# Kernel tuning notes

Hardware: AMD Instinct MI355X
Metric: run time of the kernel (lower is better)

The kernel has to match this reference:

```python
import jax, jax.numpy as jnp
import numpy as np

B, N, E, DIN, DOUT = 8, 4096, 160, 15, 15


def _mha(q, k, v, in_w, in_b, out_w, out_b, h):
    # torch.nn.MultiheadAttention math: packed in_proj, per-head scaled dot attn, out_proj.
    e = q.shape[-1]
    d = e // h
    scale = 1.0 / np.sqrt(d)

    def proj(x, w, b):
        y = x @ w.T + b
        return jnp.moveaxis(y.reshape(y.shape[:-1] + (h, d)), -2, -3)  # [..., h, L, d]

    qh = proj(q, in_w[:e], in_b[:e])
    kh = proj(k, in_w[e:2 * e], in_b[e:2 * e])
    vh = proj(v, in_w[2 * e:], in_b[2 * e:])
    a = jax.nn.softmax(jnp.einsum('...hld,...hmd->...hlm', qh, kh) * scale, axis=-1)
    o = jnp.einsum('...hlm,...hmd->...hld', a, vh)
    o = jnp.moveaxis(o, -3, -2).reshape(q.shape)
    return o @ out_w.T + out_b


def _attn_layer(seq, Wq, Wk, Wv, in_w, in_b, out_w, out_b, h):
    # AttentionLayer: extra Wq/Wk/Wv projections feeding the MHA
    return _mha(seq @ Wq, seq @ Wk, seq @ Wv, in_w, in_b, out_w, out_b, h)


def setup_inputs():
    key = jax.random.key(0)
    ks = jax.random.split(key, 20)
    s = 1.0 / np.sqrt(E)
    p = lambda i, shape: jax.random.normal(ks[i], shape, dtype=jnp.float32) * s
    return {
        'X_batch': jax.random.normal(ks[0], (B, N, E), dtype=jnp.float32),
        'in_idx': jax.random.randint(ks[1], (B, N, DIN), 0, N),
        'out_idx': jax.random.randint(ks[2], (B, N, DOUT), 0, N),
        'iWq': p(3, (E, E)), 'iWk': p(4, (E, E)), 'iWv': p(5, (E, E)),
        'i_in_w': p(6, (3 * E, E)), 'i_in_b': jnp.zeros(3 * E, jnp.float32),
        'i_out_w': p(7, (E, E)), 'i_out_b': jnp.zeros(E, jnp.float32),
        'oWq': p(8, (E, E)), 'oWk': p(9, (E, E)), 'oWv': p(10, (E, E)),
        'o_in_w': p(11, (3 * E, E)), 'o_in_b': jnp.zeros(3 * E, jnp.float32),
        'o_out_w': p(12, (E, E)), 'o_out_b': jnp.zeros(E, jnp.float32),
        'f_in_w': p(13, (3 * E, E)), 'f_in_b': jnp.zeros(3 * E, jnp.float32),
        'f_out_w': p(14, (E, E)), 'f_out_b': jnp.zeros(E, jnp.float32),
        'lin_w': p(15, (E, E)), 'lin_b': jnp.zeros(E, jnp.float32),
    }


def reference(X_batch, in_idx, out_idx,
              iWq, iWk, iWv, i_in_w, i_in_b, i_out_w, i_out_b,
              oWq, oWk, oWv, o_in_w, o_in_b, o_out_w, o_out_b,
              f_in_w, f_in_b, f_out_w, f_out_b, lin_w, lin_b):
    b_ix = jnp.arange(X_batch.shape[0])[:, None, None]
    self_f = X_batch[:, :, None, :]                                   # [B,N,1,E]
    seq_in = jnp.concatenate([self_f, X_batch[b_ix, in_idx]], axis=2)  # [B,N,1+DIN,E]
    seq_out = jnp.concatenate([self_f, X_batch[b_ix, out_idx]], axis=2)
    a_in = _attn_layer(seq_in, iWq, iWk, iWv, i_in_w, i_in_b, i_out_w, i_out_b, 5)
    a_out = _attn_layer(seq_out, oWq, oWk, oWv, o_in_w, o_in_b, o_out_w, o_out_b, 5)
    a = jnp.concatenate([a_in, a_out], axis=2)                         # [B,N,2+DIN+DOUT,E]
    f = _mha(a, a, a, f_in_w, f_in_b, f_out_w, f_out_b, 1)
    pooled = jnp.max(f, axis=2)                                        # max over sequence dim
    return jax.nn.elu(pooled @ lin_w.T + lin_b)
```

## Files before the change

kernel.cpp:

```cpp
#include <hip/hip_runtime.h>
#include <hip/hip_bf16.h>
#include <math.h>

#define NTH 256

typedef __bf16 bf16x8 __attribute__((ext_vector_type(8)));
typedef float  f32x4  __attribute__((ext_vector_type(4)));
typedef unsigned short ushort;
typedef ushort u16x8 __attribute__((ext_vector_type(8)));

__device__ __forceinline__ ushort f2bf(float x){
    union { float f; unsigned int u; } v; v.f = x;
    unsigned int r = v.u + 0x7fffu + ((v.u >> 16) & 1u);
    return (ushort)(r >> 16);
}
__device__ __forceinline__ float bf2f(ushort h){
    union { unsigned int u; float f; } v; v.u = ((unsigned int)h) << 16;
    return v.f;
}

__global__ void prep_combined_bf(const float* __restrict__ Wq, const float* __restrict__ Wk,
                                 const float* __restrict__ Wv, const float* __restrict__ in_w,
                                 ushort* __restrict__ dh)
{
    int o = blockIdx.x*NTH + threadIdx.x;
    if (o >= 76800) return;
    int c = o/160, j = o - c*160;
    const float* Wsel = (c<160) ? Wq : (c<320) ? Wk : Wv;
    const float* wrow = Wsel + j*160;
    const float* irow = in_w + c*160;
    float s = 0.f;
    for (int k=0;k<160;k++) s = fmaf(wrow[k], irow[k], s);
    dh[o] = f2bf(s);
}

__global__ void prep_H_split(const float* __restrict__ f_in_w, const float* __restrict__ out_w,
                             ushort* __restrict__ dh, float* __restrict__ tmp)
{
    int o = blockIdx.x*NTH + threadIdx.x;
    if (o >= 76800) return;
    int n = o/160, k = o - n*160;
    float s = 0.f;
    for (int c=0;c<160;c++) s = fmaf(f_in_w[n*160+c], out_w[c*160+k], s);
    if (n < 320) dh[o] = f2bf(s);
    else         tmp[(n-320)*160 + k] = s;
}

__global__ void prep_H_fold(const float* __restrict__ fo, const float* __restrict__ Hv,
                            ushort* __restrict__ dh)
{
    int o = blockIdx.x*NTH + threadIdx.x;
    if (o >= 25600) return;
    int n = o/160, k = o - n*160;
    float s = 0.f;
    for (int j=0;j<160;j++) s = fmaf(fo[n*160+j], Hv[j*160+k], s);
    dh[(320+n)*160 + k] = f2bf(s);
}

__global__ void prep_cvec(const float* __restrict__ f_in_w, const float* __restrict__ out_b,
                          const float* __restrict__ f_in_b, float* __restrict__ cvt)
{
    int n = blockIdx.x*NTH + threadIdx.x;
    if (n >= 480) return;
    float s = f_in_b[n];
    for (int c=0;c<160;c++) s = fmaf(f_in_w[n*160+c], out_b[c], s);
    cvt[n] = s;
}

__global__ void prep_cvec_fold(const float* __restrict__ fo, const float* __restrict__ cvt,
                               float* __restrict__ cv)
{
    int n = blockIdx.x*NTH + threadIdx.x;
    if (n >= 480) return;
    if (n < 320){ cv[n] = cvt[n]; return; }
    int m = n - 320;
    float s = 0.f;
    for (int j=0;j<160;j++) s = fmaf(fo[m*160+j], cvt[320+j], s);
    cv[n] = s;
}

__global__ void prep_conv_bf1(const float* __restrict__ src, ushort* __restrict__ dh, int n)
{
    int o = blockIdx.x*NTH + threadIdx.x;
    if (o >= n) return;
    dh[o] = f2bf(src[o]);
}

__global__ void prep_conv_bf2(const float* __restrict__ src,
                              ushort* __restrict__ dh, ushort* __restrict__ dl, int n)
{
    int o = blockIdx.x*NTH + threadIdx.x;
    if (o >= n) return;
    float s = src[o];
    ushort h = f2bf(s);
    dh[o] = h; dl[o] = f2bf(s - bf2f(h));
}

__global__ __launch_bounds__(NTH)
void gemm_mfma_lin(const float* __restrict__ A,
                   const ushort* __restrict__ Wh, const ushort* __restrict__ Wl,
                   const float* __restrict__ bias, float* __restrict__ C, int N)
{
    __shared__ ushort sAh[128*40], sAl[128*40];
    __shared__ ushort sWh[160*40], sWl[160*40];

    const int tid = threadIdx.x;
    const int lane = tid & 63, wave = tid >> 6;
    const int wm = wave >> 1, wn = wave & 1;
    const int ln = lane & 15, g = lane >> 4;
    const long m0 = (long)blockIdx.x * 128;
    const int  n0 = blockIdx.y * 160;

    f32x4 acc[4][5];
#pragma unroll
    for (int mt=0;mt<4;mt++)
#pragma unroll
        for (int nt=0;nt<5;nt++)
#pragma unroll
            for (int r=0;r<4;r++) acc[mt][nt][r] = 0.f;

    for (int k0=0;k0<160;k0+=32){
#pragma unroll
        for (int i=0;i<4;i++){
            int f = tid + 256*i;
            int m = f >> 3, seg = f & 7;
            float4 v = *(const float4*)(A + (m0+m)*160 + k0 + seg*4);
            ushort4 hv, lv;
            hv.x = f2bf(v.x); lv.x = f2bf(v.x - bf2f(hv.x));
            hv.y = f2bf(v.y); lv.y = f2bf(v.y - bf2f(hv.y));
            hv.z = f2bf(v.z); lv.z = f2bf(v.z - bf2f(hv.z));
            hv.w = f2bf(v.w); lv.w = f2bf(v.w - bf2f(hv.w));
            *(ushort4*)(sAh + m*40 + seg*4) = hv;
            *(ushort4*)(sAl + m*40 + seg*4) = lv;
        }
#pragma unroll
        for (int i=0;i<5;i++){
            int e = tid + 256*i;
            int pl = (e >= 640);
            int idx = pl ? e-640 : e;
            int n = idx >> 2, seg = idx & 3;
            const ushort* src = (pl ? Wl : Wh) + (long)(n0+n)*160 + k0 + seg*8;
            ushort* dst = (pl ? sWl : sWh) + n*40 + seg*8;
            *(uint4*)dst = *(const uint4*)src;
        }
        __syncthreads();

        bf16x8 ah[4], al[4];
#pragma unroll
        for (int mt=0;mt<4;mt++){
            int off = (wm*64 + mt*16 + ln)*40 + g*8;
            ah[mt] = *(const bf16x8*)(sAh + off);
            al[mt] = *(const bf16x8*)(sAl + off);
        }
#pragma unroll
        for (int nt=0;nt<5;nt++){
            int offw = (wn*80 + nt*16 + ln)*40 + g*8;
            bf16x8 bh = *(const bf16x8*)(sWh + offw);
            bf16x8 bl = *(const bf16x8*)(sWl + offw);
#pragma unroll
            for (int mt=0;mt<4;mt++){
                acc[mt][nt] = __builtin_amdgcn_mfma_f32_16x16x32_bf16(ah[mt], bh, acc[mt][nt], 0,0,0);
                acc[mt][nt] = __builtin_amdgcn_mfma_f32_16x16x32_bf16(al[mt], bh, acc[mt][nt], 0,0,0);
                acc[mt][nt] = __builtin_amdgcn_mfma_f32_16x16x32_bf16(ah[mt], bl, acc[mt][nt], 0,0,0);
            }
        }
        __syncthreads();
    }

#pragma unroll
    for (int nt=0;nt<5;nt++){
        int col = n0 + wn*80 + nt*16 + ln;
        float bv = bias[col];
#pragma unroll
        for (int mt=0;mt<4;mt++){
#pragma unroll
            for (int r=0;r<4;r++){
                long row = m0 + wm*64 + mt*16 + g*4 + r;
                float x = acc[mt][nt][r] + bv;
                x = x > 0.f ? x : expm1f(x);
                C[row*N + col] = x;
            }
        }
    }
}

__global__ __launch_bounds__(NTH)
void gemm_bf(const ushort* __restrict__ A0, const ushort* __restrict__ A1,
             const ushort* __restrict__ Wh0, const ushort* __restrict__ Wh1,
             const float* __restrict__ b0, const float* __restrict__ b1,
             ushort* __restrict__ C0, ushort* __restrict__ C1, int N)
{
    const int z = blockIdx.z;
    const ushort* A  = z ? A1 : A0;
    const ushort* Wh = z ? Wh1 : Wh0;
    const float* bias = z ? b1 : b0;
    ushort* C = z ? C1 : C0;

    __shared__ ushort sA[128*40];
    __shared__ ushort sW[160*40];

    const int tid = threadIdx.x;
    const int lane = tid & 63, wave = tid >> 6;
    const int wm = wave >> 1, wn = wave & 1;
    const int ln = lane & 15, g = lane >> 4;
    const long m0 = (long)blockIdx.x * 128;
    const int  n0 = blockIdx.y * 160;

    f32x4 acc[4][5];
#pragma unroll
    for (int mt=0;mt<4;mt++)
#pragma unroll
        for (int nt=0;nt<5;nt++)
#pragma unroll
            for (int r=0;r<4;r++) acc[mt][nt][r] = 0.f;

    for (int k0=0;k0<160;k0+=32){
#pragma unroll
        for (int i=0;i<2;i++){
            int e = tid + 256*i;
            int m = e >> 2, seg = e & 3;
            *(uint4*)(sA + m*40 + seg*8) =
                *(const uint4*)(A + (m0+m)*160 + k0 + seg*8);
        }
#pragma unroll
        for (int i=0;i<3;i++){
            int e = tid + 256*i;
            if (e < 640){
                int n = e >> 2, seg = e & 3;
                *(uint4*)(sW + n*40 + seg*8) =
                    *(const uint4*)(Wh + (long)(n0+n)*160 + k0 + seg*8);
            }
        }
        __syncthreads();

        bf16x8 af[4];
#pragma unroll
        for (int mt=0;mt<4;mt++)
            af[mt] = *(const bf16x8*)(sA + (wm*64 + mt*16 + ln)*40 + g*8);
#pragma unroll
        for (int nt=0;nt<5;nt++){
            bf16x8 bh = *(const bf16x8*)(sW + (wn*80 + nt*16 + ln)*40 + g*8);
#pragma unroll
            for (int mt=0;mt<4;mt++)
                acc[mt][nt] = __builtin_amdgcn_mfma_f32_16x16x32_bf16(af[mt], bh, acc[mt][nt], 0,0,0);
        }
        __syncthreads();
    }

#pragma unroll
    for (int nt=0;nt<5;nt++){
        int col = n0 + wn*80 + nt*16 + ln;
        float bv = bias[col];
#pragma unroll
        for (int mt=0;mt<4;mt++){
#pragma unroll
            for (int r=0;r<4;r++){
                long row = m0 + wm*64 + mt*16 + g*4 + r;
                C[row*N + col] = f2bf(acc[mt][nt][r] + bv);
            }
        }
    }
}

__global__ __launch_bounds__(64)
void attn_layer_mfma(const ushort* __restrict__ XPi, const ushort* __restrict__ XPo,
                     const int* __restrict__ in_idx, const int* __restrict__ out_idx,
                     ushort* __restrict__ Oi, ushort* __restrict__ Oo, int node_base)
{
    const ushort* XP = blockIdx.y ? XPo : XPi;
    const int*  idx  = blockIdx.y ? out_idx : in_idx;
    ushort* O        = blockIdx.y ? Oo : Oi;

    __shared__ ushort XPg[16*496];
    __shared__ ushort Pall[5*16*24];

    const int lane = threadIdx.x;
    const int ln = lane & 15, q = lane >> 4;
    const int node = node_base + blockIdx.x;
    const int bb = node >> 12, nn = node & 4095;

    int idxv = nn;
    if (lane >= 1 && lane < 16) idxv = idx[(long)node*15 + lane-1];

#pragma unroll
    for (int i=0;i<15;i++){
        int e = lane + 64*i;
        int r = e/60, c = e - r*60;
        int rowg = __shfl(idxv, r);
        *(uint4*)(XPg + r*496 + c*8) =
            *(const uint4*)(XP + (long)(bb*4096 + rowg)*480 + c*8);
    }
    __syncthreads();

    const float scale = 0.17677669529663687f;
#pragma unroll
    for (int h=0;h<5;h++){
        bf16x8 ka = *(const bf16x8*)(XPg + ln*496 + 160 + h*32 + q*8);
        bf16x8 qb = *(const bf16x8*)(XPg + ln*496 +       h*32 + q*8);
        f32x4 s = {0.f,0.f,0.f,0.f};
        s = __builtin_amdgcn_mfma_f32_16x16x32_bf16(ka, qb, s, 0,0,0);
        float x[4], m = -1e30f;
#pragma unroll
        for (int r=0;r<4;r++){ x[r] = s[r]*scale; m = fmaxf(m, x[r]); }
        m = fmaxf(m, __shfl_xor(m, 16));
        m = fmaxf(m, __shfl_xor(m, 32));
        float e0[4], sum = 0.f;
#pragma unroll
        for (int r=0;r<4;r++){ e0[r] = __expf(x[r]-m); sum += e0[r]; }
        sum += __shfl_xor(sum, 16);
        sum += __shfl_xor(sum, 32);
        float inv = 1.f/sum;
        ushort4 pw;
        pw.x = f2bf(e0[0]*inv); pw.y = f2bf(e0[1]*inv);
        pw.z = f2bf(e0[2]*inv); pw.w = f2bf(e0[3]*inv);
        *(ushort4*)(Pall + h*384 + ln*24 + q*4) = pw;
    }
    __syncthreads();

#pragma unroll
    for (int h=0;h<5;h++){
        u16x8 ta;
#pragma unroll
        for (int jj=0;jj<8;jj++) ta[jj] = 0;
        if (q < 2) ta = *(const u16x8*)(Pall + h*384 + ln*24 + q*8);
        bf16x8 ap = *(bf16x8*)&ta;
#pragma unroll
        for (int half=0; half<2; half++){
            u16x8 tb;
#pragma unroll
            for (int jj=0;jj<8;jj++) tb[jj] = 0;
            if (q < 2){
#pragma unroll
                for (int jj=0;jj<8;jj++)
                    tb[jj] = XPg[(q*8+jj)*496 + 320 + h*32 + half*16 + ln];
            }
            bf16x8 bv = *(bf16x8*)&tb;
            f32x4 o = {0.f,0.f,0.f,0.f};
            o = __builtin_amdgcn_mfma_f32_16x16x32_bf16(ap, bv, o, 0,0,0);
#pragma unroll
            for (int r=0;r<4;r++)
                O[(long)(blockIdx.x*16 + q*4 + r)*160 + h*32 + half*16 + ln] = f2bf(o[r]);
        }
    }
}

__global__ __launch_bounds__(512)
void fused_fq_attn_pool(const ushort* __restrict__ O_i, const ushort* __restrict__ O_o,
                        const ushort* __restrict__ Hi, const ushort* __restrict__ Ho,
                        const float* __restrict__ c_i, const float* __restrict__ c_o,
                        const float* __restrict__ fb, float* __restrict__ pooled,
                        int node_base)
{
    __shared__ ushort sFQ[4*32*328];
    __shared__ ushort sVt[4*160*40];
    __shared__ ushort sP [4*32*40];

    const int tid  = threadIdx.x;
    const int lane = tid & 63, wave = tid >> 6;
    const int ln = lane & 15, g = lane >> 4;
    const int wl = wave >> 2, wn = wave & 3;
    const int nl0 = blockIdx.x * 4;

    const ushort* Ow = wl ? O_o : O_i;
    const ushort* Hw = wl ? Ho  : Hi;
    const float*  cw = wl ? c_o : c_i;

    bf16x8 ofr[4][5];
#pragma unroll
    for (int nd=0; nd<4; nd++)
#pragma unroll
        for (int kc=0; kc<5; kc++)
            ofr[nd][kc] = *(const bf16x8*)(Ow + ((long)(nl0+nd)*16 + ln)*160 + kc*32 + g*8);

    bf16x8 hf[5], hn[5];
#pragma unroll
    for (int kc=0; kc<5; kc++)
        hf[kc] = *(const bf16x8*)(Hw + (long)(wn*16 + ln)*160 + kc*32 + g*8);

    for (int t=0; t<8; t++){
        const int cg  = t*4 + wn;
        const int cgn = cg + 4;
        if (t < 7 && cgn < 30){
            const ushort* hrow = Hw + (long)(cgn*16 + ln)*160;
#pragma unroll
            for (int kc=0; kc<5; kc++)
                hn[kc] = *(const bf16x8*)(hrow + kc*32 + g*8);
        }

        if (cg < 30){
            f32x4 acc[4];
#pragma unroll
            for (int nd=0; nd<4; nd++)
#pragma unroll
                for (int r=0;r<4;r++) acc[nd][r] = 0.f;

#pragma unroll
            for (int kc=0; kc<5; kc++)
#pragma unroll
                for (int nd=0; nd<4; nd++)
                    acc[nd] = __builtin_amdgcn_mfma_f32_16x16x32_bf16(hf[kc], ofr[nd][kc], acc[nd], 0,0,0);

            const int cb0 = cg*16 + g*4;
            float4 cb = *(const float4*)(cw + cb0);
            if (cg < 20){
#pragma unroll
                for (int nd=0; nd<4; nd++){
                    ushort4 w4;
                    w4.x = f2bf(acc[nd][0] + cb.x);
                    w4.y = f2bf(acc[nd][1] + cb.y);
                    w4.z = f2bf(acc[nd][2] + cb.z);
                    w4.w = f2bf(acc[nd][3] + cb.w);
                    *(ushort4*)(sFQ + nd*10496 + (wl*16 + ln)*328 + cb0) = w4;
                }
            } else {
                const int c0 = cb0 - 320;
#pragma unroll
                for (int nd=0; nd<4; nd++){
                    sVt[nd*6400 + (c0+0)*40 + wl*16 + ln] = f2bf(acc[nd][0] + cb.x);
                    sVt[nd*6400 + (c0+1)*40 + wl*16 + ln] = f2bf(acc[nd][1] + cb.y);
                    sVt[nd*6400 + (c0+2)*40 + wl*16 + ln] = f2bf(acc[nd][2] + cb.z);
                    sVt[nd*6400 + (c0+3)*40 + wl*16 + ln] = f2bf(acc[nd][3] + cb.w);
                }
            }
        }
#pragma unroll
        for (int kc=0; kc<5; kc++) hf[kc] = hn[kc];
    }
    __syncthreads();

    const int nd = wave >> 1, th = wave & 1;
    const ushort* myQ = sFQ + nd*10496;
    const ushort* myV = sVt + nd*6400;
    ushort*       myP = sP  + nd*1280;

    f32x4 sc[2];
#pragma unroll
    for (int tj=0; tj<2; tj++){
        f32x4 a = {0.f,0.f,0.f,0.f};
#pragma unroll
        for (int kc=0; kc<5; kc++){
            bf16x8 ka = *(const bf16x8*)(myQ + (tj*16+ln)*328 + 160 + kc*32 + g*8);
            bf16x8 qb = *(const bf16x8*)(myQ + (th*16+ln)*328 +       kc*32 + g*8);
            a = __builtin_amdgcn_mfma_f32_16x16x32_bf16(ka, qb, a, 0,0,0);
        }
        sc[tj] = a;
    }

    const float scale = 0.07905694150420949f;
    {
        float x[2][4], m = -1e30f;
#pragma unroll
        for (int tj=0; tj<2; tj++)
#pragma unroll
            for (int r=0;r<4;r++){ x[tj][r] = sc[tj][r]*scale; m = fmaxf(m, x[tj][r]); }
        m = fmaxf(m, __shfl_xor(m, 16));
        m = fmaxf(m, __shfl_xor(m, 32));
        float sum = 0.f;
#pragma unroll
        for (int tj=0; tj<2; tj++)
#pragma unroll
            for (int r=0;r<4;r++){ x[tj][r] = __expf(x[tj][r]-m); sum += x[tj][r]; }
        sum += __shfl_xor(sum, 16);
        sum += __shfl_xor(sum, 32);
        float inv = 1.f/sum;
#pragma unroll
        for (int tj=0; tj<2; tj++){
            ushort4 pw;
            pw.x = f2bf(x[tj][0]*inv); pw.y = f2bf(x[tj][1]*inv);
            pw.z = f2bf(x[tj][2]*inv); pw.w = f2bf(x[tj][3]*inv);
            *(ushort4*)(myP + (th*16+ln)*40 + tj*16 + g*4) = pw;
        }
    }
    __syncthreads();

    bf16x8 ap[2];
#pragma unroll
    for (int mi=0; mi<2; mi++)
        ap[mi] = *(const bf16x8*)(myP + (mi*16+ln)*40 + g*8);

    const long node = (long)node_base + nl0 + nd;
#pragma unroll
    for (int nt5=0; nt5<5; nt5++){
        const int nt = th*5 + nt5;
        bf16x8 bv = *(const bf16x8*)(myV + (nt*16+ln)*40 + g*8);
        float vmax = -1e30f;
#pragma unroll
        for (int mi=0; mi<2; mi++){
            f32x4 o = {0.f,0.f,0.f,0.f};
            o = __builtin_amdgcn_mfma_f32_16x16x32_bf16(ap[mi], bv, o, 0,0,0);
#pragma unroll
            for (int r=0;r<4;r++) vmax = fmaxf(vmax, o[r]);
        }
        vmax = fmaxf(vmax, __shfl_xor(vmax, 16));
        vmax = fmaxf(vmax, __shfl_xor(vmax, 32));
        if (g == 0){
            int col = nt*16 + ln;
            pooled[node*160 + col] = vmax + fb[col];
        }
    }
}

extern "C" void kernel_launch(void* const* d_in, const int* in_sizes, int n_in,
                              void* d_out, int out_size, void* d_ws, size_t ws_size,
                              hipStream_t stream)
{
    const float* X       = (const float*)d_in[0];
    const int*   in_idx  = (const int*)  d_in[1];
    const int*   out_idx = (const int*)  d_in[2];
    const float* iWq     = (const float*)d_in[3];
    const float* iWk     = (const float*)d_in[4];
    const float* iWv     = (const float*)d_in[5];
    const float* i_in_w  = (const float*)d_in[6];
    const float* i_in_b  = (const float*)d_in[7];
    const float* i_out_w = (const float*)d_in[8];
    const float* i_out_b = (const float*)d_in[9];
    const float* oWq     = (const float*)d_in[10];
    const float* oWk     = (const float*)d_in[11];
    const float* oWv     = (const float*)d_in[12];
    const float* o_in_w  = (const float*)d_in[13];
    const float* o_in_b  = (const float*)d_in[14];
    const float* o_out_w = (const float*)d_in[15];
    const float* o_out_b = (const float*)d_in[16];
    const float* f_in_w  = (const float*)d_in[17];
    const float* f_in_b  = (const float*)d_in[18];
    const float* f_out_w = (const float*)d_in[19];
    const float* f_out_b = (const float*)d_in[20];
    const float* lin_w   = (const float*)d_in[21];
    const float* lin_b   = (const float*)d_in[22];

    float* ws = (float*)d_ws;
    float* pooled = ws;
    float* c_i    = pooled + 5242880;
    float* c_o    = c_i + 480;
    float* cvt_i  = c_o + 480;
    float* cvt_o  = cvt_i + 480;
    float* Hvt_i  = cvt_o + 480;
    float* Hvt_o  = Hvt_i + 25600;
    ushort* ub    = (ushort*)(Hvt_o + 25600);
    ushort* Xb    = ub;
    ushort* XPb_i = Xb + 5242880;
    ushort* XPb_o = XPb_i + 15728640;
    ushort* Wci_h = XPb_o + 15728640;
    ushort* Wco_h = Wci_h + 76800;
    ushort* Hi_h  = Wco_h + 76800;
    ushort* Ho_h  = Hi_h  + 76800;
    ushort* li_h  = Ho_h  + 76800;
    ushort* li_l  = li_h  + 25600;
    ushort* sb_us = li_l + 25600;
    const unsigned long long fixed = 23825280ULL;

    size_t avail = ws_size / 4;
    int ns = 32768;
    while (ns > 64 && fixed + 2560ULL*ns > avail) ns >>= 1;

    ushort* O_i = sb_us;
    ushort* O_o = O_i + (size_t)2560*ns;

    prep_combined_bf<<<300,NTH,0,stream>>>(iWq,iWk,iWv,i_in_w, Wci_h);
    prep_combined_bf<<<300,NTH,0,stream>>>(oWq,oWk,oWv,o_in_w, Wco_h);
    prep_H_split<<<300,NTH,0,stream>>>(f_in_w, i_out_w, Hi_h, Hvt_i);
    prep_H_split<<<300,NTH,0,stream>>>(f_in_w, o_out_w, Ho_h, Hvt_o);
    prep_H_fold<<<100,NTH,0,stream>>>(f_out_w, Hvt_i, Hi_h);
    prep_H_fold<<<100,NTH,0,stream>>>(f_out_w, Hvt_o, Ho_h);
    prep_cvec<<<2,NTH,0,stream>>>(f_in_w, i_out_b, f_in_b, cvt_i);
    prep_cvec<<<2,NTH,0,stream>>>(f_in_w, o_out_b, f_in_b, cvt_o);
    prep_cvec_fold<<<2,NTH,0,stream>>>(f_out_w, cvt_i, c_i);
    prep_cvec_fold<<<2,NTH,0,stream>>>(f_out_w, cvt_o, c_o);
    prep_conv_bf2<<<100,NTH,0,stream>>>(lin_w, li_h, li_l, 25600);
    prep_conv_bf1<<<20480,NTH,0,stream>>>(X, Xb, 5242880);

    dim3 g1(256, 3, 2);
    gemm_bf<<<g1,NTH,0,stream>>>(Xb, Xb, Wci_h, Wco_h, i_in_b, o_in_b,
                                 XPb_i, XPb_o, 480);

    int S = 32768 / ns;
    for (int s=0;s<S;s++){
        int base = s*ns;
        dim3 ga(ns, 2);
        attn_layer_mfma<<<ga,64,0,stream>>>(XPb_i, XPb_o, in_idx, out_idx, O_i, O_o, base);
        fused_fq_attn_pool<<<ns/4,512,0,stream>>>(O_i, O_o, Hi_h, Ho_h, c_i, c_o,
                                                  f_out_b, pooled, base);
    }

    dim3 g6(256, 1);
    gemm_mfma_lin<<<g6,NTH,0,stream>>>(pooled, li_h, li_l, lin_b, (float*)d_out, 160);
}
```

Baseline: 764.6 us.

## Fuse per-node attention layers and final attention-pool into one mega kernel

Merges the per-node gather+5-head attention kernel and the fused F/Q attention-pool kernel into a single 1024-thread block that handles 4 nodes. The intermediate O tensors now stay in LDS instead of going through global memory, and the out-layer gather is prefetched into registers while the in-layer is computed. The chunked launch loop and its O workspace are removed. The cost is a large LDS footprint (about 142 KB) and 1024-thread blocks, which limit occupancy to one block per CU, and half the waves sit idle in the final attention stage.

```diff
diff --git a/kernel.cpp b/kernel.cpp
--- a/kernel.cpp
+++ b/kernel.cpp
@@ -262,106 +262,133 @@
     }
 }
 
-__global__ __launch_bounds__(64)
-void attn_layer_mfma(const ushort* __restrict__ XPi, const ushort* __restrict__ XPo,
-                     const int* __restrict__ in_idx, const int* __restrict__ out_idx,
-                     ushort* __restrict__ Oi, ushort* __restrict__ Oo, int node_base)
-{
-    const ushort* XP = blockIdx.y ? XPo : XPi;
-    const int*  idx  = blockIdx.y ? out_idx : in_idx;
-    ushort* O        = blockIdx.y ? Oo : Oi;
-
-    __shared__ ushort XPg[16*496];
-    __shared__ ushort Pall[5*16*24];
-
-    const int lane = threadIdx.x;
-    const int ln = lane & 15, q = lane >> 4;
-    const int node = node_base + blockIdx.x;
-    const int bb = node >> 12, nn = node & 4095;
-
-    int idxv = nn;
-    if (lane >= 1 && lane < 16) idxv = idx[(long)node*15 + lane-1];
-
-#pragma unroll
-    for (int i=0;i<15;i++){
-        int e = lane + 64*i;
-        int r = e/60, c = e - r*60;
-        int rowg = __shfl(idxv, r);
-        *(uint4*)(XPg + r*496 + c*8) =
-            *(const uint4*)(XP + (long)(bb*4096 + rowg)*480 + c*8);
+__global__ __launch_bounds__(1024)
+void mega_node(const ushort* __restrict__ XPi, const ushort* __restrict__ XPo,
+               const int* __restrict__ in_idx, const int* __restrict__ out_idx,
+               const ushort* __restrict__ Hi, const ushort* __restrict__ Ho,
+               const float* __restrict__ c_i, const float* __restrict__ c_o,
+               const float* __restrict__ fb, float* __restrict__ pooled)
+{
+    __shared__ ushort lds[72704];
+
+    const int tid  = threadIdx.x;
+    const int lane = tid & 63, w = tid >> 6;
+    const int ln = lane & 15, g = lane >> 4;
+    const int nl0 = blockIdx.x * 4;
+
+    ushort* XPg = lds;
+    ushort* sO  = lds + 31744;
+    ushort* sPh = lds + 53248;
+
+    const int ndA = w & 3, p = w >> 2;
+    const int nodeA = nl0 + ndA;
+    const int bb = nodeA >> 12, nn = nodeA & 4095;
+    int idx0 = nn, idx1 = nn;
+    if (lane >= 1 && lane < 16){
+        idx0 = in_idx [(long)nodeA*15 + lane-1];
+        idx1 = out_idx[(long)nodeA*15 + lane-1];
+    }
+
+    uint4 l1r[4];
+#pragma unroll
+    for (int i=0;i<4;i++){
+        int e = i*256 + p*64 + lane;
+        if (e < 960){
+            int r = e/60, c = e - r*60;
+            int rowg = __shfl(idx0, r);
+            *(uint4*)(XPg + ndA*7936 + r*496 + c*8) =
+                *(const uint4*)(XPi + (long)(bb*4096 + rowg)*480 + c*8);
+        }
+    }
+#pragma unroll
+    for (int i=0;i<4;i++){
+        int e = i*256 + p*64 + lane;
+        if (e < 960){
+            int r = e/60, c = e - r*60;
+            int rowg = __shfl(idx1, r);
+            l1r[i] = *(const uint4*)(XPo + (long)(bb*4096 + rowg)*480 + c*8);
+        }
     }
     __syncthreads();
 
-    const float scale = 0.17677669529663687f;
-#pragma unroll
-    for (int h=0;h<5;h++){
-        bf16x8 ka = *(const bf16x8*)(XPg + ln*496 + 160 + h*32 + q*8);
-        bf16x8 qb = *(const bf16x8*)(XPg + ln*496 +       h*32 + q*8);
-        f32x4 s = {0.f,0.f,0.f,0.f};
-        s = __builtin_amdgcn_mfma_f32_16x16x32_bf16(ka, qb, s, 0,0,0);
-        float x[4], m = -1e30f;
-#pragma unroll
-        for (int r=0;r<4;r++){ x[r] = s[r]*scale; m = fmaxf(m, x[r]); }
-        m = fmaxf(m, __shfl_xor(m, 16));
-        m = fmaxf(m, __shfl_xor(m, 32));
-        float e0[4], sum = 0.f;
-#pragma unroll
-        for (int r=0;r<4;r++){ e0[r] = __expf(x[r]-m); sum += e0[r]; }
-        sum += __shfl_xor(sum, 16);
-        sum += __shfl_xor(sum, 32);
-        float inv = 1.f/sum;
-        ushort4 pw;
-        pw.x = f2bf(e0[0]*inv); pw.y = f2bf(e0[1]*inv);
-        pw.z = f2bf(e0[2]*inv); pw.w = f2bf(e0[3]*inv);
-        *(ushort4*)(Pall + h*384 + ln*24 + q*4) = pw;
-    }
-    __syncthreads();
-
-#pragma unroll
-    for (int h=0;h<5;h++){
-        u16x8 ta;
-#pragma unroll
-        for (int jj=0;jj<8;jj++) ta[jj] = 0;
-        if (q < 2) ta = *(const u16x8*)(Pall + h*384 + ln*24 + q*8);
-        bf16x8 ap = *(bf16x8*)&ta;
-#pragma unroll
-        for (int half=0; half<2; half++){
-            u16x8 tb;
-#pragma unroll
-            for (int jj=0;jj<8;jj++) tb[jj] = 0;
-            if (q < 2){
-#pragma unroll
-                for (int jj=0;jj<8;jj++)
-                    tb[jj] = XPg[(q*8+jj)*496 + 320 + h*32 + half*16 + ln];
-            }
-            bf16x8 bv = *(bf16x8*)&tb;
-            f32x4 o = {0.f,0.f,0.f,0.f};
-            o = __builtin_amdgcn_mfma_f32_16x16x32_bf16(ap, bv, o, 0,0,0);
-#pragma unroll
-            for (int r=0;r<4;r++)
-                O[(long)(blockIdx.x*16 + q*4 + r)*160 + h*32 + half*16 + ln] = f2bf(o[r]);
-        }
-    }
-}
-
-__global__ __launch_bounds__(512)
-void fused_fq_attn_pool(const ushort* __restrict__ O_i, const ushort* __restrict__ O_o,
-                        const ushort* __restrict__ Hi, const ushort* __restrict__ Ho,
-                        const float* __restrict__ c_i, const float* __restrict__ c_o,
-                        const float* __restrict__ fb, float* __restrict__ pooled,
-                        int node_base)
-{
-    __shared__ ushort sFQ[4*32*328];
-    __shared__ ushort sVt[4*160*40];
-    __shared__ ushort sP [4*32*40];
-
-    const int tid  = threadIdx.x;
-    const int lane = tid & 63, wave = tid >> 6;
-    const int ln = lane & 15, g = lane >> 4;
-    const int wl = wave >> 2, wn = wave & 3;
-    const int nl0 = blockIdx.x * 4;
-
-    const ushort* Ow = wl ? O_o : O_i;
+    const float scale1 = 0.17677669529663687f;
+#pragma unroll
+    for (int l=0; l<2; l++){
+        if (l == 1){
+#pragma unroll
+            for (int i=0;i<4;i++){
+                int e = i*256 + p*64 + lane;
+                if (e < 960){
+                    int r = e/60, c = e - r*60;
+                    *(uint4*)(XPg + ndA*7936 + r*496 + c*8) = l1r[i];
+                }
+            }
+            __syncthreads();
+        }
+
+#pragma unroll
+        for (int rep=0; rep<2; rep++){
+            int t = w + rep*16;
+            if (t < 20){
+                int nd = t/5, h = t - 5*(t/5);
+                const ushort* xg = XPg + nd*7936;
+                bf16x8 ka = *(const bf16x8*)(xg + ln*496 + 160 + h*32 + g*8);
+                bf16x8 qb = *(const bf16x8*)(xg + ln*496 +       h*32 + g*8);
+                f32x4 s = {0.f,0.f,0.f,0.f};
+                s = __builtin_amdgcn_mfma_f32_16x16x32_bf16(ka, qb, s, 0,0,0);
+                float x[4], m = -1e30f;
+#pragma unroll
+                for (int r=0;r<4;r++){ x[r] = s[r]*scale1; m = fmaxf(m, x[r]); }
+                m = fmaxf(m, __shfl_xor(m, 16));
+                m = fmaxf(m, __shfl_xor(m, 32));
+                float e0[4], sum = 0.f;
+#pragma unroll
+                for (int r=0;r<4;r++){ e0[r] = __expf(x[r]-m); sum += e0[r]; }
+                sum += __shfl_xor(sum, 16);
+                sum += __shfl_xor(sum, 32);
+                float inv = 1.f/sum;
+                ushort4 pw;
+                pw.x = f2bf(e0[0]*inv); pw.y = f2bf(e0[1]*inv);
+                pw.z = f2bf(e0[2]*inv); pw.w = f2bf(e0[3]*inv);
+                *(ushort4*)(sPh + t*384 + ln*24 + g*4) = pw;
+            }
+        }
+        __syncthreads();
+
+#pragma unroll
+        for (int rep=0; rep<2; rep++){
+            int t = w + rep*16;
+            if (t < 20){
+                int nd = t/5, h = t - 5*(t/5);
+                const ushort* xg = XPg + nd*7936;
+                u16x8 ta;
+#pragma unroll
+                for (int jj=0;jj<8;jj++) ta[jj] = 0;
+                if (g < 2) ta = *(const u16x8*)(sPh + t*384 + ln*24 + g*8);
+                bf16x8 ap = *(bf16x8*)&ta;
+#pragma unroll
+                for (int half=0; half<2; half++){
+                    u16x8 tb;
+#pragma unroll
+                    for (int jj=0;jj<8;jj++) tb[jj] = 0;
+                    if (g < 2){
+#pragma unroll
+                        for (int jj=0;jj<8;jj++)
+                            tb[jj] = xg[(g*8+jj)*496 + 320 + h*32 + half*16 + ln];
+                    }
+                    bf16x8 bv = *(bf16x8*)&tb;
+                    f32x4 o = {0.f,0.f,0.f,0.f};
+                    o = __builtin_amdgcn_mfma_f32_16x16x32_bf16(ap, bv, o, 0,0,0);
+#pragma unroll
+                    for (int r=0;r<4;r++)
+                        sO[((nd*2+l)*16 + g*4+r)*168 + h*32 + half*16 + ln] = f2bf(o[r]);
+                }
+            }
+        }
+        __syncthreads();
+    }
+
+    const int wl = w >> 3, wn = w & 7;
     const ushort* Hw = wl ? Ho  : Hi;
     const float*  cw = wl ? c_o : c_i;
 
@@ -370,21 +397,28 @@
     for (int nd=0; nd<4; nd++)
 #pragma unroll
         for (int kc=0; kc<5; kc++)
-            ofr[nd][kc] = *(const bf16x8*)(Ow + ((long)(nl0+nd)*16 + ln)*160 + kc*32 + g*8);
+            ofr[nd][kc] = *(const bf16x8*)(sO + ((nd*2+wl)*16 + ln)*168 + kc*32 + g*8);
 
     bf16x8 hf[5], hn[5];
 #pragma unroll
     for (int kc=0; kc<5; kc++)
         hf[kc] = *(const bf16x8*)(Hw + (long)(wn*16 + ln)*160 + kc*32 + g*8);
-
-    for (int t=0; t<8; t++){
-        const int cg  = t*4 + wn;
-        const int cgn = cg + 4;
-        if (t < 7 && cgn < 30){
-            const ushort* hrow = Hw + (long)(cgn*16 + ln)*160;
-#pragma unroll
-            for (int kc=0; kc<5; kc++)
-                hn[kc] = *(const bf16x8*)(hrow + kc*32 + g*8);
+    __syncthreads();
+
+    ushort* sFQ = lds;
+    ushort* sVt = lds + 41984;
+    ushort* sPf = lds + 67584;
+
+    for (int t=0; t<4; t++){
+        const int cg = t*8 + wn;
+        if (t < 3){
+            const int cgn = cg + 8;
+            if (cgn < 30){
+                const ushort* hrow = Hw + (long)(cgn*16 + ln)*160;
+#pragma unroll
+                for (int kc=0; kc<5; kc++)
+                    hn[kc] = *(const bf16x8*)(hrow + kc*32 + g*8);
+            }
         }
 
         if (cg < 30){
@@ -428,26 +462,26 @@
     }
     __syncthreads();
 
-    const int nd = wave >> 1, th = wave & 1;
+    const int nd = w >> 1, th = w & 1;
     const ushort* myQ = sFQ + nd*10496;
     const ushort* myV = sVt + nd*6400;
-    ushort*       myP = sP  + nd*1280;
-
-    f32x4 sc[2];
-#pragma unroll
-    for (int tj=0; tj<2; tj++){
-        f32x4 a = {0.f,0.f,0.f,0.f};
-#pragma unroll
-        for (int kc=0; kc<5; kc++){
-            bf16x8 ka = *(const bf16x8*)(myQ + (tj*16+ln)*328 + 160 + kc*32 + g*8);
-            bf16x8 qb = *(const bf16x8*)(myQ + (th*16+ln)*328 +       kc*32 + g*8);
-            a = __builtin_amdgcn_mfma_f32_16x16x32_bf16(ka, qb, a, 0,0,0);
-        }
-        sc[tj] = a;
-    }
-
-    const float scale = 0.07905694150420949f;
-    {
+    ushort*       myP = sPf + nd*1280;
+
+    if (w < 8){
+        f32x4 sc[2];
+#pragma unroll
+        for (int tj=0; tj<2; tj++){
+            f32x4 a = {0.f,0.f,0.f,0.f};
+#pragma unroll
+            for (int kc=0; kc<5; kc++){
+                bf16x8 ka = *(const bf16x8*)(myQ + (tj*16+ln)*328 + 160 + kc*32 + g*8);
+                bf16x8 qb = *(const bf16x8*)(myQ + (th*16+ln)*328 +       kc*32 + g*8);
+                a = __builtin_amdgcn_mfma_f32_16x16x32_bf16(ka, qb, a, 0,0,0);
+            }
+            sc[tj] = a;
+        }
+
+        const float scale = 0.07905694150420949f;
         float x[2][4], m = -1e30f;
 #pragma unroll
         for (int tj=0; tj<2; tj++)
@@ -473,29 +507,31 @@
     }
     __syncthreads();
 
-    bf16x8 ap[2];
-#pragma unroll
-    for (int mi=0; mi<2; mi++)
-        ap[mi] = *(const bf16x8*)(myP + (mi*16+ln)*40 + g*8);
-
-    const long node = (long)node_base + nl0 + nd;
-#pragma unroll
-    for (int nt5=0; nt5<5; nt5++){
-        const int nt = th*5 + nt5;
-        bf16x8 bv = *(const bf16x8*)(myV + (nt*16+ln)*40 + g*8);
-        float vmax = -1e30f;
-#pragma unroll
-        for (int mi=0; mi<2; mi++){
-            f32x4 o = {0.f,0.f,0.f,0.f};
-            o = __builtin_amdgcn_mfma_f32_16x16x32_bf16(ap[mi], bv, o, 0,0,0);
-#pragma unroll
-            for (int r=0;r<4;r++) vmax = fmaxf(vmax, o[r]);
-        }
-        vmax = fmaxf(vmax, __shfl_xor(vmax, 16));
-        vmax = fmaxf(vmax, __shfl_xor(vmax, 32));
-        if (g == 0){
-            int col = nt*16 + ln;
-            pooled[node*160 + col] = vmax + fb[col];
+    if (w < 8){
+        bf16x8 ap[2];
+#pragma unroll
+        for (int mi=0; mi<2; mi++)
+            ap[mi] = *(const bf16x8*)(myP + (mi*16+ln)*40 + g*8);
+
+        const long node = (long)nl0 + nd;
+#pragma unroll
+        for (int nt5=0; nt5<5; nt5++){
+            const int nt = th*5 + nt5;
+            bf16x8 bv = *(const bf16x8*)(myV + (nt*16+ln)*40 + g*8);
+            float vmax = -1e30f;
+#pragma unroll
+            for (int mi=0; mi<2; mi++){
+                f32x4 o = {0.f,0.f,0.f,0.f};
+                o = __builtin_amdgcn_mfma_f32_16x16x32_bf16(ap[mi], bv, o, 0,0,0);
+#pragma unroll
+                for (int r=0;r<4;r++) vmax = fmaxf(vmax, o[r]);
+            }
+            vmax = fmaxf(vmax, __shfl_xor(vmax, 16));
+            vmax = fmaxf(vmax, __shfl_xor(vmax, 32));
+            if (g == 0){
+                int col = nt*16 + ln;
+                pooled[node*160 + col] = vmax + fb[col];
+            }
         }
     }
 }
@@ -536,8 +572,7 @@
     float* cvt_o  = cvt_i + 480;
     float* Hvt_i  = cvt_o + 480;
     float* Hvt_o  = Hvt_i + 25600;
-    ushort* ub    = (ushort*)(Hvt_o + 25600);
-    ushort* Xb    = ub;
+    ushort* Xb    = (ushort*)(Hvt_o + 25600);
     ushort* XPb_i = Xb + 5242880;
     ushort* XPb_o = XPb_i + 15728640;
     ushort* Wci_h = XPb_o + 15728640;
@@ -546,15 +581,6 @@
     ushort* Ho_h  = Hi_h  + 76800;
     ushort* li_h  = Ho_h  + 76800;
     ushort* li_l  = li_h  + 25600;
-    ushort* sb_us = li_l + 25600;
-    const unsigned long long fixed = 23825280ULL;
-
-    size_t avail = ws_size / 4;
-    int ns = 32768;
-    while (ns > 64 && fixed + 2560ULL*ns > avail) ns >>= 1;
-
-    ushort* O_i = sb_us;
-    ushort* O_o = O_i + (size_t)2560*ns;
 
     prep_combined_bf<<<300,NTH,0,stream>>>(iWq,iWk,iWv,i_in_w, Wci_h);
     prep_combined_bf<<<300,NTH,0,stream>>>(oWq,oWk,oWv,o_in_w, Wco_h);
@@ -573,14 +599,8 @@
     gemm_bf<<<g1,NTH,0,stream>>>(Xb, Xb, Wci_h, Wco_h, i_in_b, o_in_b,
                                  XPb_i, XPb_o, 480);
 
-    int S = 32768 / ns;
-    for (int s=0;s<S;s++){
-        int base = s*ns;
-        dim3 ga(ns, 2);
-        attn_layer_mfma<<<ga,64,0,stream>>>(XPb_i, XPb_o, in_idx, out_idx, O_i, O_o, base);
-        fused_fq_attn_pool<<<ns/4,512,0,stream>>>(O_i, O_o, Hi_h, Ho_h, c_i, c_o,
-                                                  f_out_b, pooled, base);
-    }
+    mega_node<<<8192,1024,0,stream>>>(XPb_i, XPb_o, in_idx, out_idx,
+                                      Hi_h, Ho_h, c_i, c_o, f_out_b, pooled);
 
     dim3 g6(256, 1);
     gemm_mfma_lin<<<g6,NTH,0,stream>>>(pooled, li_h, li_l, lin_b, (float*)d_out, 160);
```

Result: slower. 1.126 ms (+47.2%).
